# Kernel optimization log

Hardware: AMD Instinct MI355X
Metric: run time of the kernel (lower is better)

The kernel has to match this reference:

```python
import jax, jax.numpy as jnp
import numpy as np

NTYPE = 3
ALPHA = 0.2
E, N, H, D = 100000, 50000, 4, 128


def setup_inputs() -> dict:
    key = jax.random.key(0)
    k1, k2, k3 = jax.random.split(key, 3)
    batch = jax.random.randint(k1, (E, NTYPE), 0, N)
    # forward's broadcast (batch_features + aggregated) requires every node id
    # to appear at least once (torch.unique(batch) must have N entries)
    batch = batch.at[:N, 0].set(jnp.arange(N))
    batch_features = jax.random.normal(k2, (N, D), dtype=jnp.float32)
    att_weights = jax.random.normal(k3, (NTYPE * E, H, NTYPE - 1), dtype=jnp.float32)
    return {"batch": batch, "batch_features": batch_features, "att_weights": att_weights}


def reference(batch, batch_features, att_weights):
    n_nodes, d = batch_features.shape
    # feat block i: gather embeddings of all type-columns except i -> [NTYPE*E, NTYPE-1, D]
    feat = jnp.concatenate(
        [batch_features[batch[:, [j for j in range(NTYPE) if j != i]]] for i in range(NTYPE)],
        axis=0,
    )
    # batched attention matmul: [NTYPE*E, H, NTYPE-1] x [NTYPE*E, NTYPE-1, D] -> [NTYPE*E, H, D]
    att_feat = jnp.einsum('ehk,ekd->ehd', att_weights, feat)
    # block i of att_feat corresponds to node ids batch[:, i] (matches batch.T.flatten())
    batch_nodes = batch.T.reshape(-1)  # [NTYPE*E]
    # per-node scatter-max aggregation (torch.unique returns sorted ids 0..N-1)
    aggregated = jax.ops.segment_max(att_feat, batch_nodes, num_segments=n_nodes)  # [N, H, D]
    out = batch_features[:, None, :] + aggregated  # broadcast residual -> [N, H, D]
    out = jax.nn.leaky_relu(out, negative_slope=ALPHA)  # concat=True branch
    return out.reshape(n_nodes, -1)  # [N, H*D]
```

## Files before the change

kernel.cpp:

```cpp
#include <hip/hip_runtime.h>

#define NTYPE 3
#define H 4
#define D 128
#define ALPHA 0.2f

#define SCAN_TILE 1024

typedef float f2 __attribute__((ext_vector_type(2)));
typedef float f4 __attribute__((ext_vector_type(4)));

__global__ void count_kernel(const int* __restrict__ batch,
                             int* __restrict__ cnt,
                             int* __restrict__ rnk, int E) {
    int r = blockIdx.x * blockDim.x + threadIdx.x;
    if (r >= E) return;
    const int* row = batch + 3 * r;
    int b0 = row[0], b1 = row[1], b2 = row[2];
    rnk[r]         = atomicAdd(&cnt[b0], 1);
    rnk[E + r]     = atomicAdd(&cnt[b1], 1);
    rnk[2 * E + r] = atomicAdd(&cnt[b2], 1);
}

__global__ void __launch_bounds__(256)
bscan_kernel(int* __restrict__ cnt, int* __restrict__ bsum, int N) {
    __shared__ int lds[256];
    const int tid = threadIdx.x;
    const int base = blockIdx.x * SCAN_TILE + tid * 4;

    int4 v = make_int4(0, 0, 0, 0);
    if (base + 3 < N) v = *(const int4*)(cnt + base);
    else {
        if (base + 0 < N) v.x = cnt[base + 0];
        if (base + 1 < N) v.y = cnt[base + 1];
        if (base + 2 < N) v.z = cnt[base + 2];
        if (base + 3 < N) v.w = cnt[base + 3];
    }
    const int s = v.x + v.y + v.z + v.w;

    lds[tid] = s;
    __syncthreads();
    for (int off = 1; off < 256; off <<= 1) {
        int t = (tid >= off) ? lds[tid - off] : 0;
        __syncthreads();
        lds[tid] += t;
        __syncthreads();
    }
    const int excl = lds[tid] - s;
    if (tid == 255) bsum[blockIdx.x] = lds[255];

    int4 o;
    o.x = excl;
    o.y = excl + v.x;
    o.z = excl + v.x + v.y;
    o.w = excl + v.x + v.y + v.z;
    if (base + 3 < N) *(int4*)(cnt + base) = o;
    else {
        if (base + 0 < N) cnt[base + 0] = o.x;
        if (base + 1 < N) cnt[base + 1] = o.y;
        if (base + 2 < N) cnt[base + 2] = o.z;
        if (base + 3 < N) cnt[base + 3] = o.w;
    }
}

__global__ void __launch_bounds__(256)
add_kernel(int* __restrict__ cnt, const int* __restrict__ bsum, int N) {
    __shared__ int off_s;
    const int tid = threadIdx.x;
    if (tid < 64) {
        int acc = 0;
        for (int i = tid; i < (int)blockIdx.x; i += 64) acc += bsum[i];
        for (int o = 32; o > 0; o >>= 1) acc += __shfl_down(acc, o);
        if (tid == 0) off_s = acc;
    }
    __syncthreads();
    const int off = off_s;

    const int base = blockIdx.x * SCAN_TILE + tid * 4;
    if (base + 3 < N) {
        int4 v = *(int4*)(cnt + base);
        v.x += off; v.y += off; v.z += off; v.w += off;
        *(int4*)(cnt + base) = v;
    } else {
        for (int i = 0; i < 4; ++i)
            if (base + i < N) cnt[base + i] += off;
    }
}

__global__ void scatter_kernel(const int* __restrict__ batch,
                               const int* __restrict__ start,
                               const int* __restrict__ rnk,
                               int4* __restrict__ recs, int E) {
    int r = blockIdx.x * blockDim.x + threadIdx.x;
    if (r >= E) return;
    const int* row = batch + 3 * r;
    int b0 = row[0], b1 = row[1], b2 = row[2];
    int s0 = start[b0] + rnk[r];
    int s1 = start[b1] + rnk[E + r];
    int s2 = start[b2] + rnk[2 * E + r];
    recs[s0] = make_int4(b1, b2, r, 0);
    recs[s1] = make_int4(b0, b2, E + r, 0);
    recs[s2] = make_int4(b0, b1, 2 * E + r, 0);
}

__global__ void __launch_bounds__(64)
aggregate_kernel(const float* __restrict__ bfeat,
                 const float* __restrict__ attw,
                 const int4* __restrict__ recs,
                 const int* __restrict__ cursor,
                 float* __restrict__ out, int M) {
    const int n = blockIdx.x;
    const int t = threadIdx.x;
    const int s = cursor[n];
    const int e = (n == (int)gridDim.x - 1) ? M : cursor[n + 1];

    const float NI = -__builtin_inff();
    f2 acc0 = {NI, NI}, acc1 = {NI, NI}, acc2 = {NI, NI}, acc3 = {NI, NI};

    int k = s;
    for (; k + 2 <= e; k += 2) {
        const int4 ra = recs[k];
        const int4 rb = recs[k + 1];
        const f2 fa0 = *(const f2*)(bfeat + (size_t)ra.x * D + 2 * t);
        const f2 fa1 = *(const f2*)(bfeat + (size_t)ra.y * D + 2 * t);
        const f2 fb0 = *(const f2*)(bfeat + (size_t)rb.x * D + 2 * t);
        const f2 fb1 = *(const f2*)(bfeat + (size_t)rb.y * D + 2 * t);
        const f4 wa0 = *(const f4*)(attw + (size_t)ra.z * 8);
        const f4 wa1 = *(const f4*)(attw + (size_t)ra.z * 8 + 4);
        const f4 wb0 = *(const f4*)(attw + (size_t)rb.z * 8);
        const f4 wb1 = *(const f4*)(attw + (size_t)rb.z * 8 + 4);

        acc0.x = fmaxf(acc0.x, fmaf(wa0.x, fa0.x, wa0.y * fa1.x));
        acc0.y = fmaxf(acc0.y, fmaf(wa0.x, fa0.y, wa0.y * fa1.y));
        acc1.x = fmaxf(acc1.x, fmaf(wa0.z, fa0.x, wa0.w * fa1.x));
        acc1.y = fmaxf(acc1.y, fmaf(wa0.z, fa0.y, wa0.w * fa1.y));
        acc2.x = fmaxf(acc2.x, fmaf(wa1.x, fa0.x, wa1.y * fa1.x));
        acc2.y = fmaxf(acc2.y, fmaf(wa1.x, fa0.y, wa1.y * fa1.y));
        acc3.x = fmaxf(acc3.x, fmaf(wa1.z, fa0.x, wa1.w * fa1.x));
        acc3.y = fmaxf(acc3.y, fmaf(wa1.z, fa0.y, wa1.w * fa1.y));

        acc0.x = fmaxf(acc0.x, fmaf(wb0.x, fb0.x, wb0.y * fb1.x));
        acc0.y = fmaxf(acc0.y, fmaf(wb0.x, fb0.y, wb0.y * fb1.y));
        acc1.x = fmaxf(acc1.x, fmaf(wb0.z, fb0.x, wb0.w * fb1.x));
        acc1.y = fmaxf(acc1.y, fmaf(wb0.z, fb0.y, wb0.w * fb1.y));
        acc2.x = fmaxf(acc2.x, fmaf(wb1.x, fb0.x, wb1.y * fb1.x));
        acc2.y = fmaxf(acc2.y, fmaf(wb1.x, fb0.y, wb1.y * fb1.y));
        acc3.x = fmaxf(acc3.x, fmaf(wb1.z, fb0.x, wb1.w * fb1.x));
        acc3.y = fmaxf(acc3.y, fmaf(wb1.z, fb0.y, wb1.w * fb1.y));
    }
    if (k < e) {
        const int4 ra = recs[k];
        const f2 fa0 = *(const f2*)(bfeat + (size_t)ra.x * D + 2 * t);
        const f2 fa1 = *(const f2*)(bfeat + (size_t)ra.y * D + 2 * t);
        const f4 wa0 = *(const f4*)(attw + (size_t)ra.z * 8);
        const f4 wa1 = *(const f4*)(attw + (size_t)ra.z * 8 + 4);
        acc0.x = fmaxf(acc0.x, fmaf(wa0.x, fa0.x, wa0.y * fa1.x));
        acc0.y = fmaxf(acc0.y, fmaf(wa0.x, fa0.y, wa0.y * fa1.y));
        acc1.x = fmaxf(acc1.x, fmaf(wa0.z, fa0.x, wa0.w * fa1.x));
        acc1.y = fmaxf(acc1.y, fmaf(wa0.z, fa0.y, wa0.w * fa1.y));
        acc2.x = fmaxf(acc2.x, fmaf(wa1.x, fa0.x, wa1.y * fa1.x));
        acc2.y = fmaxf(acc2.y, fmaf(wa1.x, fa0.y, wa1.y * fa1.y));
        acc3.x = fmaxf(acc3.x, fmaf(wa1.z, fa0.x, wa1.w * fa1.x));
        acc3.y = fmaxf(acc3.y, fmaf(wa1.z, fa0.y, wa1.w * fa1.y));
    }

    const f2 br = *(const f2*)(bfeat + (size_t)n * D + 2 * t);
    float* o = out + (size_t)n * (H * D) + 2 * t;
    f2 v;

    v.x = br.x + acc0.x; v.y = br.y + acc0.y;
    v.x = v.x > 0.f ? v.x : ALPHA * v.x; v.y = v.y > 0.f ? v.y : ALPHA * v.y;
    __builtin_nontemporal_store(v, (f2*)(o + 0 * D));

    v.x = br.x + acc1.x; v.y = br.y + acc1.y;
    v.x = v.x > 0.f ? v.x : ALPHA * v.x; v.y = v.y > 0.f ? v.y : ALPHA * v.y;
    __builtin_nontemporal_store(v, (f2*)(o + 1 * D));

    v.x = br.x + acc2.x; v.y = br.y + acc2.y;
    v.x = v.x > 0.f ? v.x : ALPHA * v.x; v.y = v.y > 0.f ? v.y : ALPHA * v.y;
    __builtin_nontemporal_store(v, (f2*)(o + 2 * D));

    v.x = br.x + acc3.x; v.y = br.y + acc3.y;
    v.x = v.x > 0.f ? v.x : ALPHA * v.x; v.y = v.y > 0.f ? v.y : ALPHA * v.y;
    __builtin_nontemporal_store(v, (f2*)(o + 3 * D));
}

extern "C" void kernel_launch(void* const* d_in, const int* in_sizes, int n_in,
                              void* d_out, int out_size, void* d_ws, size_t ws_size,
                              hipStream_t stream) {
    const int* batch   = (const int*)d_in[0];
    const float* bfeat = (const float*)d_in[1];
    const float* attw  = (const float*)d_in[2];
    const int E = in_sizes[0] / NTYPE;
    const int N = in_sizes[1] / D;
    const int M = NTYPE * E;

    int* cursor = (int*)d_ws;
    size_t rec_off = (((size_t)N * sizeof(int)) + 15) & ~(size_t)15;
    int4* recs = (int4*)((char*)d_ws + rec_off);
    int* bsum = (int*)recs;
    int* rnk  = (int*)d_out;

    const int nb = (N + SCAN_TILE - 1) / SCAN_TILE;

    hipMemsetAsync(cursor, 0, sizeof(int) * (size_t)N, stream);
    count_kernel<<<(E + 255) / 256, 256, 0, stream>>>(batch, cursor, rnk, E);
    bscan_kernel<<<nb, 256, 0, stream>>>(cursor, bsum, N);
    add_kernel<<<nb, 256, 0, stream>>>(cursor, bsum, N);
    scatter_kernel<<<(E + 255) / 256, 256, 0, stream>>>(batch, cursor, rnk, recs, E);
    aggregate_kernel<<<N, 64, 0, stream>>>(bfeat, attw, recs, cursor, (float*)d_out, M);
}
```

Baseline: 196.4 us.

## Fuse CSR build stages into one cooperative kernel with grid syncs

Replaces the memset, count, block-scan, add and scatter launches with a single cooperative kernel of 512x256 threads that uses grid-wide syncs between phases. The goal is to remove per-launch overhead and the gaps between the small preprocessing kernels. The aggregate kernel also switches its record and attention-weight loads to nontemporal loads to reduce cache pollution. The cost is that cooperative grid syncs add their own overhead, and the grid-stride loops run with fewer threads than the separate launches did.

```diff
diff --git a/kernel.cpp b/kernel.cpp
--- a/kernel.cpp
+++ b/kernel.cpp
@@ -1,4 +1,7 @@
 #include <hip/hip_runtime.h>
+#include <hip/hip_cooperative_groups.h>
+
+namespace cg = cooperative_groups;
 
 #define NTYPE 3
 #define H 4
@@ -9,98 +12,100 @@
 
 typedef float f2 __attribute__((ext_vector_type(2)));
 typedef float f4 __attribute__((ext_vector_type(4)));
-
-__global__ void count_kernel(const int* __restrict__ batch,
-                             int* __restrict__ cnt,
-                             int* __restrict__ rnk, int E) {
-    int r = blockIdx.x * blockDim.x + threadIdx.x;
-    if (r >= E) return;
-    const int* row = batch + 3 * r;
-    int b0 = row[0], b1 = row[1], b2 = row[2];
-    rnk[r]         = atomicAdd(&cnt[b0], 1);
-    rnk[E + r]     = atomicAdd(&cnt[b1], 1);
-    rnk[2 * E + r] = atomicAdd(&cnt[b2], 1);
-}
+typedef int   i4 __attribute__((ext_vector_type(4)));
 
 __global__ void __launch_bounds__(256)
-bscan_kernel(int* __restrict__ cnt, int* __restrict__ bsum, int N) {
+build_kernel(const int* __restrict__ batch,
+             int* __restrict__ cursor,
+             int4* __restrict__ recs,
+             int* __restrict__ rnk,
+             int E, int N) {
+    cg::grid_group grid = cg::this_grid();
+    const int tid  = blockIdx.x * blockDim.x + threadIdx.x;
+    const int nthr = gridDim.x * blockDim.x;
+    int* bsum = (int*)recs;
+
+    for (int i = tid; i < N; i += nthr) cursor[i] = 0;
+    grid.sync();
+
+    for (int r = tid; r < E; r += nthr) {
+        const int* row = batch + 3 * r;
+        int b0 = row[0], b1 = row[1], b2 = row[2];
+        rnk[r]         = atomicAdd(&cursor[b0], 1);
+        rnk[E + r]     = atomicAdd(&cursor[b1], 1);
+        rnk[2 * E + r] = atomicAdd(&cursor[b2], 1);
+    }
+    grid.sync();
+
     __shared__ int lds[256];
-    const int tid = threadIdx.x;
-    const int base = blockIdx.x * SCAN_TILE + tid * 4;
-
-    int4 v = make_int4(0, 0, 0, 0);
-    if (base + 3 < N) v = *(const int4*)(cnt + base);
-    else {
-        if (base + 0 < N) v.x = cnt[base + 0];
-        if (base + 1 < N) v.y = cnt[base + 1];
-        if (base + 2 < N) v.z = cnt[base + 2];
-        if (base + 3 < N) v.w = cnt[base + 3];
-    }
-    const int s = v.x + v.y + v.z + v.w;
-
-    lds[tid] = s;
-    __syncthreads();
-    for (int off = 1; off < 256; off <<= 1) {
-        int t = (tid >= off) ? lds[tid - off] : 0;
+    const int nb = (N + SCAN_TILE - 1) / SCAN_TILE;
+    const int t  = threadIdx.x;
+    if ((int)blockIdx.x < nb) {
+        const int base = blockIdx.x * SCAN_TILE + t * 4;
+        int4 v = make_int4(0, 0, 0, 0);
+        if (base + 3 < N) v = *(const int4*)(cursor + base);
+        else {
+            if (base + 0 < N) v.x = cursor[base + 0];
+            if (base + 1 < N) v.y = cursor[base + 1];
+            if (base + 2 < N) v.z = cursor[base + 2];
+        }
+        const int s = v.x + v.y + v.z + v.w;
+        lds[t] = s;
         __syncthreads();
-        lds[tid] += t;
+        for (int off = 1; off < 256; off <<= 1) {
+            int tv = (t >= off) ? lds[t - off] : 0;
+            __syncthreads();
+            lds[t] += tv;
+            __syncthreads();
+        }
+        const int excl = lds[t] - s;
+        if (t == 255) bsum[blockIdx.x] = lds[255];
+        int4 o;
+        o.x = excl;
+        o.y = excl + v.x;
+        o.z = excl + v.x + v.y;
+        o.w = excl + v.x + v.y + v.z;
+        if (base + 3 < N) *(int4*)(cursor + base) = o;
+        else {
+            if (base + 0 < N) cursor[base + 0] = o.x;
+            if (base + 1 < N) cursor[base + 1] = o.y;
+            if (base + 2 < N) cursor[base + 2] = o.z;
+        }
+    }
+    grid.sync();
+
+    if ((int)blockIdx.x < nb) {
+        __shared__ int off_s;
+        if (t < 64) {
+            int acc = 0;
+            for (int i = t; i < (int)blockIdx.x; i += 64) acc += bsum[i];
+            for (int o = 32; o > 0; o >>= 1) acc += __shfl_down(acc, o);
+            if (t == 0) off_s = acc;
+        }
         __syncthreads();
-    }
-    const int excl = lds[tid] - s;
-    if (tid == 255) bsum[blockIdx.x] = lds[255];
-
-    int4 o;
-    o.x = excl;
-    o.y = excl + v.x;
-    o.z = excl + v.x + v.y;
-    o.w = excl + v.x + v.y + v.z;
-    if (base + 3 < N) *(int4*)(cnt + base) = o;
-    else {
-        if (base + 0 < N) cnt[base + 0] = o.x;
-        if (base + 1 < N) cnt[base + 1] = o.y;
-        if (base + 2 < N) cnt[base + 2] = o.z;
-        if (base + 3 < N) cnt[base + 3] = o.w;
-    }
-}
-
-__global__ void __launch_bounds__(256)
-add_kernel(int* __restrict__ cnt, const int* __restrict__ bsum, int N) {
-    __shared__ int off_s;
-    const int tid = threadIdx.x;
-    if (tid < 64) {
-        int acc = 0;
-        for (int i = tid; i < (int)blockIdx.x; i += 64) acc += bsum[i];
-        for (int o = 32; o > 0; o >>= 1) acc += __shfl_down(acc, o);
-        if (tid == 0) off_s = acc;
-    }
-    __syncthreads();
-    const int off = off_s;
-
-    const int base = blockIdx.x * SCAN_TILE + tid * 4;
-    if (base + 3 < N) {
-        int4 v = *(int4*)(cnt + base);
-        v.x += off; v.y += off; v.z += off; v.w += off;
-        *(int4*)(cnt + base) = v;
-    } else {
-        for (int i = 0; i < 4; ++i)
-            if (base + i < N) cnt[base + i] += off;
-    }
-}
-
-__global__ void scatter_kernel(const int* __restrict__ batch,
-                               const int* __restrict__ start,
-                               const int* __restrict__ rnk,
-                               int4* __restrict__ recs, int E) {
-    int r = blockIdx.x * blockDim.x + threadIdx.x;
-    if (r >= E) return;
-    const int* row = batch + 3 * r;
-    int b0 = row[0], b1 = row[1], b2 = row[2];
-    int s0 = start[b0] + rnk[r];
-    int s1 = start[b1] + rnk[E + r];
-    int s2 = start[b2] + rnk[2 * E + r];
-    recs[s0] = make_int4(b1, b2, r, 0);
-    recs[s1] = make_int4(b0, b2, E + r, 0);
-    recs[s2] = make_int4(b0, b1, 2 * E + r, 0);
+        const int off = off_s;
+        const int base = blockIdx.x * SCAN_TILE + t * 4;
+        if (base + 3 < N) {
+            int4 v = *(int4*)(cursor + base);
+            v.x += off; v.y += off; v.z += off; v.w += off;
+            *(int4*)(cursor + base) = v;
+        } else {
+            for (int i = 0; i < 4; ++i)
+                if (base + i < N) cursor[base + i] += off;
+        }
+    }
+    grid.sync();
+
+    for (int r = tid; r < E; r += nthr) {
+        const int* row = batch + 3 * r;
+        int b0 = row[0], b1 = row[1], b2 = row[2];
+        int s0 = cursor[b0] + rnk[r];
+        int s1 = cursor[b1] + rnk[E + r];
+        int s2 = cursor[b2] + rnk[2 * E + r];
+        recs[s0] = make_int4(b1, b2, r, 0);
+        recs[s1] = make_int4(b0, b2, E + r, 0);
+        recs[s2] = make_int4(b0, b1, 2 * E + r, 0);
+    }
 }
 
 __global__ void __launch_bounds__(64)
@@ -119,16 +124,16 @@
 
     int k = s;
     for (; k + 2 <= e; k += 2) {
-        const int4 ra = recs[k];
-        const int4 rb = recs[k + 1];
+        const i4 ra = __builtin_nontemporal_load((const i4*)(recs + k));
+        const i4 rb = __builtin_nontemporal_load((const i4*)(recs + k + 1));
         const f2 fa0 = *(const f2*)(bfeat + (size_t)ra.x * D + 2 * t);
         const f2 fa1 = *(const f2*)(bfeat + (size_t)ra.y * D + 2 * t);
         const f2 fb0 = *(const f2*)(bfeat + (size_t)rb.x * D + 2 * t);
         const f2 fb1 = *(const f2*)(bfeat + (size_t)rb.y * D + 2 * t);
-        const f4 wa0 = *(const f4*)(attw + (size_t)ra.z * 8);
-        const f4 wa1 = *(const f4*)(attw + (size_t)ra.z * 8 + 4);
-        const f4 wb0 = *(const f4*)(attw + (size_t)rb.z * 8);
-        const f4 wb1 = *(const f4*)(attw + (size_t)rb.z * 8 + 4);
+        const f4 wa0 = __builtin_nontemporal_load((const f4*)(attw + (size_t)ra.z * 8));
+        const f4 wa1 = __builtin_nontemporal_load((const f4*)(attw + (size_t)ra.z * 8 + 4));
+        const f4 wb0 = __builtin_nontemporal_load((const f4*)(attw + (size_t)rb.z * 8));
+        const f4 wb1 = __builtin_nontemporal_load((const f4*)(attw + (size_t)rb.z * 8 + 4));
 
         acc0.x = fmaxf(acc0.x, fmaf(wa0.x, fa0.x, wa0.y * fa1.x));
         acc0.y = fmaxf(acc0.y, fmaf(wa0.x, fa0.y, wa0.y * fa1.y));
@@ -149,11 +154,11 @@
         acc3.y = fmaxf(acc3.y, fmaf(wb1.z, fb0.y, wb1.w * fb1.y));
     }
     if (k < e) {
-        const int4 ra = recs[k];
+        const i4 ra = __builtin_nontemporal_load((const i4*)(recs + k));
         const f2 fa0 = *(const f2*)(bfeat + (size_t)ra.x * D + 2 * t);
         const f2 fa1 = *(const f2*)(bfeat + (size_t)ra.y * D + 2 * t);
-        const f4 wa0 = *(const f4*)(attw + (size_t)ra.z * 8);
-        const f4 wa1 = *(const f4*)(attw + (size_t)ra.z * 8 + 4);
+        const f4 wa0 = __builtin_nontemporal_load((const f4*)(attw + (size_t)ra.z * 8));
+        const f4 wa1 = __builtin_nontemporal_load((const f4*)(attw + (size_t)ra.z * 8 + 4));
         acc0.x = fmaxf(acc0.x, fmaf(wa0.x, fa0.x, wa0.y * fa1.x));
         acc0.y = fmaxf(acc0.y, fmaf(wa0.x, fa0.y, wa0.y * fa1.y));
         acc1.x = fmaxf(acc1.x, fmaf(wa0.z, fa0.x, wa0.w * fa1.x));
@@ -191,22 +196,20 @@
     const int* batch   = (const int*)d_in[0];
     const float* bfeat = (const float*)d_in[1];
     const float* attw  = (const float*)d_in[2];
-    const int E = in_sizes[0] / NTYPE;
-    const int N = in_sizes[1] / D;
-    const int M = NTYPE * E;
+    int E = in_sizes[0] / NTYPE;
+    int N = in_sizes[1] / D;
+    int M = NTYPE * E;
 
     int* cursor = (int*)d_ws;
     size_t rec_off = (((size_t)N * sizeof(int)) + 15) & ~(size_t)15;
     int4* recs = (int4*)((char*)d_ws + rec_off);
-    int* bsum = (int*)recs;
     int* rnk  = (int*)d_out;
 
-    const int nb = (N + SCAN_TILE - 1) / SCAN_TILE;
-
-    hipMemsetAsync(cursor, 0, sizeof(int) * (size_t)N, stream);
-    count_kernel<<<(E + 255) / 256, 256, 0, stream>>>(batch, cursor, rnk, E);
-    bscan_kernel<<<nb, 256, 0, stream>>>(cursor, bsum, N);
-    add_kernel<<<nb, 256, 0, stream>>>(cursor, bsum, N);
-    scatter_kernel<<<(E + 255) / 256, 256, 0, stream>>>(batch, cursor, rnk, recs, E);
-    aggregate_kernel<<<N, 64, 0, stream>>>(bfeat, attw, recs, cursor, (float*)d_out, M);
+    void* args[] = {(void*)&batch, (void*)&cursor, (void*)&recs, (void*)&rnk,
+                    (void*)&E, (void*)&N};
+    hipLaunchCooperativeKernel((const void*)build_kernel,
+                               dim3(512), dim3(256), args, 0, stream);
+
+    aggregate_kernel<<<N, 64, 0, stream>>>(bfeat, attw, recs, cursor,
+                                           (float*)d_out, M);
 }
```

New measurement: 406.0 us. 107% more time.

## Pre-permute attention weights into CSR order and fuse scan with decoupled lookback

Applied to the files above, without the earlier changes.

The separate block-scan and add kernels become a single scan kernel that uses decoupled lookback over a per-tile state array. The scatter kernel now copies each record's attention weights next to the compact neighbour indices in node-sorted order, so the aggregate kernel reads weights sequentially instead of gathering them randomly. Nontemporal loads and stores are used on the record streams. The cost moves to random 40-byte writes in the scatter step, plus a spin-wait on inter-block state in the scan; if the workspace is too small, a fallback path keeps the old indirect layout.

```diff
diff --git a/kernel.cpp b/kernel.cpp
--- a/kernel.cpp
+++ b/kernel.cpp
@@ -4,11 +4,12 @@
 #define H 4
 #define D 128
 #define ALPHA 0.2f
-
 #define SCAN_TILE 1024
 
 typedef float f2 __attribute__((ext_vector_type(2)));
 typedef float f4 __attribute__((ext_vector_type(4)));
+typedef int   i2 __attribute__((ext_vector_type(2)));
+typedef int   i4 __attribute__((ext_vector_type(4)));
 
 __global__ void count_kernel(const int* __restrict__ batch,
                              int* __restrict__ cnt,
@@ -23,10 +24,12 @@
 }
 
 __global__ void __launch_bounds__(256)
-bscan_kernel(int* __restrict__ cnt, int* __restrict__ bsum, int N) {
+scan_kernel(int* __restrict__ cnt, unsigned long long* __restrict__ tstate, int N) {
     __shared__ int lds[256];
-    const int tid = threadIdx.x;
-    const int base = blockIdx.x * SCAN_TILE + tid * 4;
+    __shared__ int excl_s;
+    const int b = blockIdx.x;
+    const int t = threadIdx.x;
+    const int base = b * SCAN_TILE + t * 4;
 
     int4 v = make_int4(0, 0, 0, 0);
     if (base + 3 < N) v = *(const int4*)(cnt + base);
@@ -34,20 +37,41 @@
         if (base + 0 < N) v.x = cnt[base + 0];
         if (base + 1 < N) v.y = cnt[base + 1];
         if (base + 2 < N) v.z = cnt[base + 2];
-        if (base + 3 < N) v.w = cnt[base + 3];
     }
     const int s = v.x + v.y + v.z + v.w;
 
-    lds[tid] = s;
+    lds[t] = s;
     __syncthreads();
     for (int off = 1; off < 256; off <<= 1) {
-        int t = (tid >= off) ? lds[tid - off] : 0;
+        int tv = (t >= off) ? lds[t - off] : 0;
         __syncthreads();
-        lds[tid] += t;
+        lds[t] += tv;
         __syncthreads();
     }
-    const int excl = lds[tid] - s;
-    if (tid == 255) bsum[blockIdx.x] = lds[255];
+    const int texcl = lds[t] - s;
+    const int tsum  = lds[255];
+
+    if (t == 0) {
+        if (b == 0) {
+            atomicExch(&tstate[0], (2ULL << 32) | (unsigned)tsum);
+            excl_s = 0;
+        } else {
+            atomicExch(&tstate[b], (1ULL << 32) | (unsigned)tsum);
+            int exclusive = 0;
+            int p = b - 1;
+            for (;;) {
+                unsigned long long st;
+                do { st = atomicAdd(&tstate[p], 0ULL); } while ((st >> 32) == 0);
+                exclusive += (int)(unsigned)st;
+                if ((st >> 32) == 2) break;
+                --p;
+            }
+            atomicExch(&tstate[b], (2ULL << 32) | (unsigned)(exclusive + tsum));
+            excl_s = exclusive;
+        }
+    }
+    __syncthreads();
+    const int excl = excl_s + texcl;
 
     int4 o;
     o.x = excl;
@@ -59,38 +83,15 @@
         if (base + 0 < N) cnt[base + 0] = o.x;
         if (base + 1 < N) cnt[base + 1] = o.y;
         if (base + 2 < N) cnt[base + 2] = o.z;
-        if (base + 3 < N) cnt[base + 3] = o.w;
-    }
-}
-
-__global__ void __launch_bounds__(256)
-add_kernel(int* __restrict__ cnt, const int* __restrict__ bsum, int N) {
-    __shared__ int off_s;
-    const int tid = threadIdx.x;
-    if (tid < 64) {
-        int acc = 0;
-        for (int i = tid; i < (int)blockIdx.x; i += 64) acc += bsum[i];
-        for (int o = 32; o > 0; o >>= 1) acc += __shfl_down(acc, o);
-        if (tid == 0) off_s = acc;
-    }
-    __syncthreads();
-    const int off = off_s;
-
-    const int base = blockIdx.x * SCAN_TILE + tid * 4;
-    if (base + 3 < N) {
-        int4 v = *(int4*)(cnt + base);
-        v.x += off; v.y += off; v.z += off; v.w += off;
-        *(int4*)(cnt + base) = v;
-    } else {
-        for (int i = 0; i < 4; ++i)
-            if (base + i < N) cnt[base + i] += off;
-    }
-}
-
-__global__ void scatter_kernel(const int* __restrict__ batch,
-                               const int* __restrict__ start,
-                               const int* __restrict__ rnk,
-                               int4* __restrict__ recs, int E) {
+    }
+}
+
+__global__ void scatter_emb_kernel(const int* __restrict__ batch,
+                                   const int* __restrict__ start,
+                                   const int* __restrict__ rnk,
+                                   const float* __restrict__ attw,
+                                   i2* __restrict__ recs,
+                                   f4* __restrict__ wrec, int E) {
     int r = blockIdx.x * blockDim.x + threadIdx.x;
     if (r >= E) return;
     const int* row = batch + 3 * r;
@@ -98,19 +99,47 @@
     int s0 = start[b0] + rnk[r];
     int s1 = start[b1] + rnk[E + r];
     int s2 = start[b2] + rnk[2 * E + r];
-    recs[s0] = make_int4(b1, b2, r, 0);
-    recs[s1] = make_int4(b0, b2, E + r, 0);
-    recs[s2] = make_int4(b0, b1, 2 * E + r, 0);
+    f4 w0a = *(const f4*)(attw + (size_t)r * 8);
+    f4 w0b = *(const f4*)(attw + (size_t)r * 8 + 4);
+    f4 w1a = *(const f4*)(attw + ((size_t)E + r) * 8);
+    f4 w1b = *(const f4*)(attw + ((size_t)E + r) * 8 + 4);
+    f4 w2a = *(const f4*)(attw + ((size_t)2 * E + r) * 8);
+    f4 w2b = *(const f4*)(attw + ((size_t)2 * E + r) * 8 + 4);
+    i2 r0; r0.x = b1; r0.y = b2;
+    i2 r1; r1.x = b0; r1.y = b2;
+    i2 r2; r2.x = b0; r2.y = b1;
+    __builtin_nontemporal_store(r0, recs + s0);
+    __builtin_nontemporal_store(w0a, wrec + 2 * (size_t)s0);
+    __builtin_nontemporal_store(w0b, wrec + 2 * (size_t)s0 + 1);
+    __builtin_nontemporal_store(r1, recs + s1);
+    __builtin_nontemporal_store(w1a, wrec + 2 * (size_t)s1);
+    __builtin_nontemporal_store(w1b, wrec + 2 * (size_t)s1 + 1);
+    __builtin_nontemporal_store(r2, recs + s2);
+    __builtin_nontemporal_store(w2a, wrec + 2 * (size_t)s2);
+    __builtin_nontemporal_store(w2b, wrec + 2 * (size_t)s2 + 1);
+}
+
+__global__ void scatter_idx_kernel(const int* __restrict__ batch,
+                                   const int* __restrict__ start,
+                                   const int* __restrict__ rnk,
+                                   int4* __restrict__ recs, int E) {
+    int r = blockIdx.x * blockDim.x + threadIdx.x;
+    if (r >= E) return;
+    const int* row = batch + 3 * r;
+    int b0 = row[0], b1 = row[1], b2 = row[2];
+    recs[start[b0] + rnk[r]]         = make_int4(b1, b2, r, 0);
+    recs[start[b1] + rnk[E + r]]     = make_int4(b0, b2, E + r, 0);
+    recs[start[b2] + rnk[2 * E + r]] = make_int4(b0, b1, 2 * E + r, 0);
 }
 
 __global__ void __launch_bounds__(64)
-aggregate_kernel(const float* __restrict__ bfeat,
-                 const float* __restrict__ attw,
-                 const int4* __restrict__ recs,
-                 const int* __restrict__ cursor,
-                 float* __restrict__ out, int M) {
+aggregate_emb_kernel(const float* __restrict__ bfeat,
+                     const i2* __restrict__ recs,
+                     const f4* __restrict__ wrec,
+                     const int* __restrict__ cursor,
+                     float* __restrict__ out, int M) {
     const int n = blockIdx.x;
-    const int t = threadIdx.x;
+    const int d2 = 2 * threadIdx.x;
     const int s = cursor[n];
     const int e = (n == (int)gridDim.x - 1) ? M : cursor[n + 1];
 
@@ -119,16 +148,16 @@
 
     int k = s;
     for (; k + 2 <= e; k += 2) {
-        const int4 ra = recs[k];
-        const int4 rb = recs[k + 1];
-        const f2 fa0 = *(const f2*)(bfeat + (size_t)ra.x * D + 2 * t);
-        const f2 fa1 = *(const f2*)(bfeat + (size_t)ra.y * D + 2 * t);
-        const f2 fb0 = *(const f2*)(bfeat + (size_t)rb.x * D + 2 * t);
-        const f2 fb1 = *(const f2*)(bfeat + (size_t)rb.y * D + 2 * t);
-        const f4 wa0 = *(const f4*)(attw + (size_t)ra.z * 8);
-        const f4 wa1 = *(const f4*)(attw + (size_t)ra.z * 8 + 4);
-        const f4 wb0 = *(const f4*)(attw + (size_t)rb.z * 8);
-        const f4 wb1 = *(const f4*)(attw + (size_t)rb.z * 8 + 4);
+        const i2 ra = __builtin_nontemporal_load(recs + k);
+        const i2 rb = __builtin_nontemporal_load(recs + k + 1);
+        const f4 wa0 = __builtin_nontemporal_load(wrec + 2 * (size_t)k);
+        const f4 wa1 = __builtin_nontemporal_load(wrec + 2 * (size_t)k + 1);
+        const f4 wb0 = __builtin_nontemporal_load(wrec + 2 * (size_t)k + 2);
+        const f4 wb1 = __builtin_nontemporal_load(wrec + 2 * (size_t)k + 3);
+        const f2 fa0 = *(const f2*)(bfeat + (size_t)ra.x * D + d2);
+        const f2 fa1 = *(const f2*)(bfeat + (size_t)ra.y * D + d2);
+        const f2 fb0 = *(const f2*)(bfeat + (size_t)rb.x * D + d2);
+        const f2 fb1 = *(const f2*)(bfeat + (size_t)rb.y * D + d2);
 
         acc0.x = fmaxf(acc0.x, fmaf(wa0.x, fa0.x, wa0.y * fa1.x));
         acc0.y = fmaxf(acc0.y, fmaf(wa0.x, fa0.y, wa0.y * fa1.y));
@@ -149,11 +178,11 @@
         acc3.y = fmaxf(acc3.y, fmaf(wb1.z, fb0.y, wb1.w * fb1.y));
     }
     if (k < e) {
-        const int4 ra = recs[k];
-        const f2 fa0 = *(const f2*)(bfeat + (size_t)ra.x * D + 2 * t);
-        const f2 fa1 = *(const f2*)(bfeat + (size_t)ra.y * D + 2 * t);
-        const f4 wa0 = *(const f4*)(attw + (size_t)ra.z * 8);
-        const f4 wa1 = *(const f4*)(attw + (size_t)ra.z * 8 + 4);
+        const i2 ra = __builtin_nontemporal_load(recs + k);
+        const f4 wa0 = __builtin_nontemporal_load(wrec + 2 * (size_t)k);
+        const f4 wa1 = __builtin_nontemporal_load(wrec + 2 * (size_t)k + 1);
+        const f2 fa0 = *(const f2*)(bfeat + (size_t)ra.x * D + d2);
+        const f2 fa1 = *(const f2*)(bfeat + (size_t)ra.y * D + d2);
         acc0.x = fmaxf(acc0.x, fmaf(wa0.x, fa0.x, wa0.y * fa1.x));
         acc0.y = fmaxf(acc0.y, fmaf(wa0.x, fa0.y, wa0.y * fa1.y));
         acc1.x = fmaxf(acc1.x, fmaf(wa0.z, fa0.x, wa0.w * fa1.x));
@@ -164,22 +193,65 @@
         acc3.y = fmaxf(acc3.y, fmaf(wa1.z, fa0.y, wa1.w * fa1.y));
     }
 
-    const f2 br = *(const f2*)(bfeat + (size_t)n * D + 2 * t);
-    float* o = out + (size_t)n * (H * D) + 2 * t;
+    const f2 br = *(const f2*)(bfeat + (size_t)n * D + d2);
+    float* o = out + (size_t)n * (H * D) + d2;
     f2 v;
-
     v.x = br.x + acc0.x; v.y = br.y + acc0.y;
     v.x = v.x > 0.f ? v.x : ALPHA * v.x; v.y = v.y > 0.f ? v.y : ALPHA * v.y;
     __builtin_nontemporal_store(v, (f2*)(o + 0 * D));
-
     v.x = br.x + acc1.x; v.y = br.y + acc1.y;
     v.x = v.x > 0.f ? v.x : ALPHA * v.x; v.y = v.y > 0.f ? v.y : ALPHA * v.y;
     __builtin_nontemporal_store(v, (f2*)(o + 1 * D));
-
     v.x = br.x + acc2.x; v.y = br.y + acc2.y;
     v.x = v.x > 0.f ? v.x : ALPHA * v.x; v.y = v.y > 0.f ? v.y : ALPHA * v.y;
     __builtin_nontemporal_store(v, (f2*)(o + 2 * D));
-
+    v.x = br.x + acc3.x; v.y = br.y + acc3.y;
+    v.x = v.x > 0.f ? v.x : ALPHA * v.x; v.y = v.y > 0.f ? v.y : ALPHA * v.y;
+    __builtin_nontemporal_store(v, (f2*)(o + 3 * D));
+}
+
+__global__ void __launch_bounds__(64)
+aggregate_idx_kernel(const float* __restrict__ bfeat,
+                     const float* __restrict__ attw,
+                     const int4* __restrict__ recs,
+                     const int* __restrict__ cursor,
+                     float* __restrict__ out, int M) {
+    const int n = blockIdx.x;
+    const int d2 = 2 * threadIdx.x;
+    const int s = cursor[n];
+    const int e = (n == (int)gridDim.x - 1) ? M : cursor[n + 1];
+
+    const float NI = -__builtin_inff();
+    f2 acc0 = {NI, NI}, acc1 = {NI, NI}, acc2 = {NI, NI}, acc3 = {NI, NI};
+
+    for (int k = s; k < e; ++k) {
+        const i4 ra = __builtin_nontemporal_load((const i4*)(recs + k));
+        const f2 fa0 = *(const f2*)(bfeat + (size_t)ra.x * D + d2);
+        const f2 fa1 = *(const f2*)(bfeat + (size_t)ra.y * D + d2);
+        const f4 wa0 = __builtin_nontemporal_load((const f4*)(attw + (size_t)ra.z * 8));
+        const f4 wa1 = __builtin_nontemporal_load((const f4*)(attw + (size_t)ra.z * 8 + 4));
+        acc0.x = fmaxf(acc0.x, fmaf(wa0.x, fa0.x, wa0.y * fa1.x));
+        acc0.y = fmaxf(acc0.y, fmaf(wa0.x, fa0.y, wa0.y * fa1.y));
+        acc1.x = fmaxf(acc1.x, fmaf(wa0.z, fa0.x, wa0.w * fa1.x));
+        acc1.y = fmaxf(acc1.y, fmaf(wa0.z, fa0.y, wa0.w * fa1.y));
+        acc2.x = fmaxf(acc2.x, fmaf(wa1.x, fa0.x, wa1.y * fa1.x));
+        acc2.y = fmaxf(acc2.y, fmaf(wa1.x, fa0.y, wa1.y * fa1.y));
+        acc3.x = fmaxf(acc3.x, fmaf(wa1.z, fa0.x, wa1.w * fa1.x));
+        acc3.y = fmaxf(acc3.y, fmaf(wa1.z, fa0.y, wa1.w * fa1.y));
+    }
+
+    const f2 br = *(const f2*)(bfeat + (size_t)n * D + d2);
+    float* o = out + (size_t)n * (H * D) + d2;
+    f2 v;
+    v.x = br.x + acc0.x; v.y = br.y + acc0.y;
+    v.x = v.x > 0.f ? v.x : ALPHA * v.x; v.y = v.y > 0.f ? v.y : ALPHA * v.y;
+    __builtin_nontemporal_store(v, (f2*)(o + 0 * D));
+    v.x = br.x + acc1.x; v.y = br.y + acc1.y;
+    v.x = v.x > 0.f ? v.x : ALPHA * v.x; v.y = v.y > 0.f ? v.y : ALPHA * v.y;
+    __builtin_nontemporal_store(v, (f2*)(o + 1 * D));
+    v.x = br.x + acc2.x; v.y = br.y + acc2.y;
+    v.x = v.x > 0.f ? v.x : ALPHA * v.x; v.y = v.y > 0.f ? v.y : ALPHA * v.y;
+    __builtin_nontemporal_store(v, (f2*)(o + 2 * D));
     v.x = br.x + acc3.x; v.y = br.y + acc3.y;
     v.x = v.x > 0.f ? v.x : ALPHA * v.x; v.y = v.y > 0.f ? v.y : ALPHA * v.y;
     __builtin_nontemporal_store(v, (f2*)(o + 3 * D));
@@ -194,19 +266,35 @@
     const int E = in_sizes[0] / NTYPE;
     const int N = in_sizes[1] / D;
     const int M = NTYPE * E;
+    const int nb = (N + SCAN_TILE - 1) / SCAN_TILE;
 
     int* cursor = (int*)d_ws;
-    size_t rec_off = (((size_t)N * sizeof(int)) + 15) & ~(size_t)15;
-    int4* recs = (int4*)((char*)d_ws + rec_off);
-    int* bsum = (int*)recs;
-    int* rnk  = (int*)d_out;
-
-    const int nb = (N + SCAN_TILE - 1) / SCAN_TILE;
-
-    hipMemsetAsync(cursor, 0, sizeof(int) * (size_t)N, stream);
-    count_kernel<<<(E + 255) / 256, 256, 0, stream>>>(batch, cursor, rnk, E);
-    bscan_kernel<<<nb, 256, 0, stream>>>(cursor, bsum, N);
-    add_kernel<<<nb, 256, 0, stream>>>(cursor, bsum, N);
-    scatter_kernel<<<(E + 255) / 256, 256, 0, stream>>>(batch, cursor, rnk, recs, E);
-    aggregate_kernel<<<N, 64, 0, stream>>>(bfeat, attw, recs, cursor, (float*)d_out, M);
-}
+    size_t off = (size_t)N * sizeof(int);
+    off = (off + 7) & ~(size_t)7;
+    unsigned long long* tstate = (unsigned long long*)((char*)d_ws + off);
+    off += (size_t)nb * 8;
+    off = (off + 15) & ~(size_t)15;
+    const size_t zero_bytes = off;
+    const size_t emb_need = off + (size_t)M * 8 + (size_t)M * 32;
+    const size_t idx_need = off + (size_t)M * 16;
+    const int eb = (E + 255) / 256;
+
+    hipMemsetAsync(d_ws, 0, zero_bytes, stream);
+    int* rnk = (int*)d_out;
+    count_kernel<<<eb, 256, 0, stream>>>(batch, cursor, rnk, E);
+    scan_kernel<<<nb, 256, 0, stream>>>(cursor, tstate, N);
+
+    if (ws_size >= emb_need) {
+        i2* recs = (i2*)((char*)d_ws + off);
+        f4* wrec = (f4*)((char*)d_ws + off + (size_t)M * 8);
+        scatter_emb_kernel<<<eb, 256, 0, stream>>>(batch, cursor, rnk, attw,
+                                                   recs, wrec, E);
+        aggregate_emb_kernel<<<N, 64, 0, stream>>>(bfeat, recs, wrec, cursor,
+                                                   (float*)d_out, M);
+    } else if (ws_size >= idx_need) {
+        int4* recs = (int4*)((char*)d_ws + off);
+        scatter_idx_kernel<<<eb, 256, 0, stream>>>(batch, cursor, rnk, recs, E);
+        aggregate_idx_kernel<<<N, 64, 0, stream>>>(bfeat, attw, recs, cursor,
+                                                   (float*)d_out, M);
+    }
+}
```

After: 221.1 us. +12.6%, slower.
